# Optimization experiments

Hardware: AMD Instinct MI355X
Metric: run time of the kernel (lower is better)

The kernel has to match this reference:

```python
import jax, jax.numpy as jnp
import numpy as np

B, N, C, H = 8, 4096, 1024, 16
D = C // H  # head_dim = 64
EPS = 1e-12

def _l2norm(x):
    # F.normalize(x, p=2, dim=-1): x / max(||x||_2, eps)
    n = jnp.sqrt(jnp.sum(x * x, axis=-1, keepdims=True))
    return x / jnp.maximum(n, EPS)

def setup_inputs() -> dict:
    key = jax.random.key(0)
    ks = jax.random.split(key, 5)
    return {
        "x": jax.random.normal(ks[0], (B, N, C), dtype=jnp.float32),
        "qkv_w": jax.random.normal(ks[1], (C, 3 * C), dtype=jnp.float32) * 0.02,
        "qkv_b": jax.random.normal(ks[2], (3 * C,), dtype=jnp.float32) * 0.02,
        "proj_w": jax.random.normal(ks[3], (C, C), dtype=jnp.float32) * 0.02,
        "proj_b": jax.random.normal(ks[4], (C,), dtype=jnp.float32) * 0.02,
    }

def reference(x, qkv_w, qkv_b, proj_w, proj_b):
    b, n, c = x.shape
    qkv = (x @ qkv_w + qkv_b).reshape(b, n, 3, H, D)
    qkv = jnp.transpose(qkv, (2, 0, 3, 1, 4))  # [3,B,H,N,D]
    q, k, v = qkv[0], qkv[1], qkv[2]
    q = _l2norm(q)
    k = _l2norm(k)
    kv = jnp.einsum('bhnd,bhne->bhde', k, v)   # small [B,H,D,D] state
    out = jnp.einsum('bhnd,bhde->bhne', q, kv)  # [B,H,N,D]
    out = jnp.transpose(out, (0, 2, 1, 3)).reshape(b, n, c)
    return out @ proj_w + proj_b
```

## Files before the change

kernel.cpp:

```cpp
#include <hip/hip_runtime.h>
#include <stdint.h>

#define B_ 8
#define N_ 4096
#define C_ 1024
#define H_ 16
#define M_ (B_*N_)
#define BH_ (B_*H_)

typedef unsigned short u16;
typedef unsigned int   u32;
typedef __bf16 bf16x8 __attribute__((ext_vector_type(8)));
typedef float  f32x4  __attribute__((ext_vector_type(4)));

__device__ __forceinline__ u16 f2bf(float f) {
  union { float f; u32 u; } x; x.f = f;
  u32 r = x.u + 0x7fffu + ((x.u >> 16) & 1u);
  return (u16)(r >> 16);
}
__device__ __forceinline__ float bf2f(u16 b) {
  union { u32 u; float f; } x; x.u = ((u32)b) << 16;
  return x.f;
}
__device__ __forceinline__ void gload16(const void* g, void* l) {
  __builtin_amdgcn_global_load_lds(
      (const __attribute__((address_space(1))) void*)g,
      (__attribute__((address_space(3))) void*)l,
      16, 0, 0);
}
__device__ __forceinline__ void unpack8(uint4 r, float* f) {
  const u32 w[4] = {r.x, r.y, r.z, r.w};
#pragma unroll
  for (int i = 0; i < 4; ++i) {
    f[2*i]   = bf2f((u16)(w[i] & 0xffffu));
    f[2*i+1] = bf2f((u16)(w[i] >> 16));
  }
}
__device__ __forceinline__ uint4 pack8(const float* f) {
  uint4 r; u32* w = (u32*)&r;
#pragma unroll
  for (int i = 0; i < 4; ++i)
    w[i] = (u32)f2bf(f[2*i]) | ((u32)f2bf(f[2*i+1]) << 16);
  return r;
}

__global__ void cast_f32_bf16(const float* __restrict__ in, u16* __restrict__ out, int n4) {
  int i = blockIdx.x * blockDim.x + threadIdx.x;
  const int stride = gridDim.x * blockDim.x;
  for (; i < n4; i += stride) {
    float4 v = reinterpret_cast<const float4*>(in)[i];
    u32 lo = (u32)f2bf(v.x) | ((u32)f2bf(v.y) << 16);
    u32 hi = (u32)f2bf(v.z) | ((u32)f2bf(v.w) << 16);
    uint2 o; o.x = lo; o.y = hi;
    reinterpret_cast<uint2*>(out)[i] = o;
  }
}

__global__ void transpose_cast(const float* __restrict__ in, u16* __restrict__ out,
                               int R, int Cc) {
  __shared__ float t[32][33];
  const int bx = blockIdx.x * 32;
  const int by = blockIdx.y * 32;
  const int tx = threadIdx.x & 31;
  const int ty = threadIdx.x >> 5;
#pragma unroll
  for (int j = 0; j < 4; ++j) {
    const int r = by + ty + j * 8;
    t[ty + j * 8][tx] = in[(size_t)r * Cc + bx + tx];
  }
  __syncthreads();
#pragma unroll
  for (int j = 0; j < 4; ++j) {
    const int c = bx + ty + j * 8;
    out[(size_t)c * R + by + tx] = f2bf(t[tx][ty + j * 8]);
  }
}

template <int NC, bool OUT_BF16>
__global__ __launch_bounds__(512) void gemm256(const u16* __restrict__ A,
                                               const u16* __restrict__ Bt,
                                               const float* __restrict__ bias,
                                               void* __restrict__ outp,
                                               int K, int cpx) {
  __shared__ __align__(16) u16 As[2][256][64];
  __shared__ __align__(16) u16 Bs[2][256][64];
  const int tid  = threadIdx.x;
  const int lane = tid & 63;
  const int w    = tid >> 6;
  const int wm   = (w >> 2) & 1;
  const int wn   = w & 3;
  const int l15  = lane & 15;
  const int lk   = lane >> 4;

  const int bid = blockIdx.x;
  const int wg  = (bid & 7) * cpx + (bid >> 3);
  const size_t brow = (size_t)(wg & 127) * 256;
  const size_t bcol = (size_t)(wg >> 7) * 256;

  const int KT = K >> 6;
  f32x4 acc[2][2][4][2] = {};

  auto stage = [&](const u16* __restrict__ src, size_t rowbase, int kt,
                   u16* lds_tile, int h) {
#pragma unroll
    for (int is = 0; is < 2; ++is) {
      const int lin   = is * 8192 + tid * 16;
      const int row   = lin >> 7;
      const int chunk = ((lin >> 4) & 7) ^ (row & 7);
      gload16(src + (rowbase + (size_t)(h * 128 + row)) * K + kt * 64 + chunk * 8,
              (char*)lds_tile + h * 16384 + lin);
    }
  };
  auto fragA = [&](const u16* tb, int mh, int mf, int kc) -> bf16x8 {
    const int row   = mh * 128 + wm * 64 + mf * 16 + l15;
    const int chunk = ((kc << 2) | lk) ^ (row & 7);
    return *reinterpret_cast<const bf16x8*>((const char*)tb + row * 128 + chunk * 16);
  };
  auto fragB = [&](const u16* tb, int nh, int nf, int kc) -> bf16x8 {
    const int row   = nh * 128 + wn * 32 + nf * 16 + l15;
    const int chunk = ((kc << 2) | lk) ^ (row & 7);
    return *reinterpret_cast<const bf16x8*>((const char*)tb + row * 128 + chunk * 16);
  };

#define MFMA_Q(AF, BF, MH, NH) do {                                            \
    __builtin_amdgcn_s_barrier();                                              \
    __builtin_amdgcn_s_setprio(1);                                             \
    _Pragma("unroll") for (int mf = 0; mf < 4; ++mf)                           \
      _Pragma("unroll") for (int nf = 0; nf < 2; ++nf)                         \
        _Pragma("unroll") for (int kc = 0; kc < 2; ++kc)                       \
          acc[MH][NH][mf][nf] = __builtin_amdgcn_mfma_f32_16x16x32_bf16(       \
              AF[mf][kc], BF[nf][kc], acc[MH][NH][mf][nf], 0, 0, 0);           \
    __builtin_amdgcn_s_setprio(0);                                             \
    __builtin_amdgcn_s_barrier();                                              \
  } while (0)

  stage(A,  brow, 0, &As[0][0][0], 0);
  stage(Bt, bcol, 0, &Bs[0][0][0], 0);
  stage(A,  brow, 0, &As[0][0][0], 1);
  stage(Bt, bcol, 0, &Bs[0][0][0], 1);
  stage(A,  brow, 1, &As[1][0][0], 0);
  stage(Bt, bcol, 1, &Bs[1][0][0], 0);
  asm volatile("s_waitcnt vmcnt(4)" ::: "memory");
  __builtin_amdgcn_s_barrier();

  for (int t = 0; t < KT; ++t) {
    const u16* curA = &As[t & 1][0][0];
    const u16* curB = &Bs[t & 1][0][0];
    u16* nA  = &As[(t + 1) & 1][0][0];
    u16* nB  = &Bs[(t + 1) & 1][0][0];
    u16* n2A = &As[t & 1][0][0];
    u16* n2B = &Bs[t & 1][0][0];
    const bool s1 = (t + 1) < KT;
    const bool s2 = (t + 2) < KT;

    bf16x8 afA[4][2], afB[4][2], bf0[2][2], bf1[2][2];

#pragma unroll
    for (int mf = 0; mf < 4; ++mf)
#pragma unroll
      for (int kc = 0; kc < 2; ++kc) afA[mf][kc] = fragA(curA, 0, mf, kc);
#pragma unroll
    for (int nf = 0; nf < 2; ++nf)
#pragma unroll
      for (int kc = 0; kc < 2; ++kc) bf0[nf][kc] = fragB(curB, 0, nf, kc);
    if (s1) stage(A, brow, t + 1, nA, 1);
    MFMA_Q(afA, bf0, 0, 0);

#pragma unroll
    for (int nf = 0; nf < 2; ++nf)
#pragma unroll
      for (int kc = 0; kc < 2; ++kc) bf1[nf][kc] = fragB(curB, 1, nf, kc);
    if (s1) stage(Bt, bcol, t + 1, nB, 1);
    MFMA_Q(afA, bf1, 0, 1);

#pragma unroll
    for (int mf = 0; mf < 4; ++mf)
#pragma unroll
      for (int kc = 0; kc < 2; ++kc) afB[mf][kc] = fragA(curA, 1, mf, kc);
    if (s2) stage(A, brow, t + 2, n2A, 0);
    MFMA_Q(afB, bf1, 1, 1);

    if (s2) {
      stage(Bt, bcol, t + 2, n2B, 0);
      asm volatile("s_waitcnt vmcnt(4)" ::: "memory");
    } else {
      asm volatile("s_waitcnt vmcnt(0)" ::: "memory");
    }
    MFMA_Q(afB, bf0, 1, 0);
  }
#undef MFMA_Q

#pragma unroll
  for (int mh = 0; mh < 2; ++mh)
#pragma unroll
  for (int nh = 0; nh < 2; ++nh)
#pragma unroll
  for (int mf = 0; mf < 4; ++mf)
#pragma unroll
  for (int nf = 0; nf < 2; ++nf) {
    const size_t col = bcol + nh * 128 + wn * 32 + nf * 16 + l15;
    const float bv = bias[col];
    const size_t row0 = brow + mh * 128 + wm * 64 + mf * 16 + lk * 4;
#pragma unroll
    for (int r = 0; r < 4; ++r) {
      const float v = acc[mh][nh][mf][nf][r] + bv;
      if constexpr (OUT_BF16)
        ((u16*)outp)[(row0 + r) * NC + col] = f2bf(v);
      else
        ((float*)outp)[(row0 + r) * NC + col] = v;
    }
  }
}

__global__ void prep(u16* __restrict__ qkv, u16* __restrict__ KT, u16* __restrict__ VT) {
  const int bh = blockIdx.x, nt = blockIdx.y;
  const int b = bh >> 4, h = bh & 15;
  const int n0 = nt * 64;
  const int tid = threadIdx.x;
  __shared__ float tk[64 * 65];

#pragma unroll
  for (int it = 0; it < 2; ++it) {
    const int idx = it * 256 + tid;
    const int r = idx >> 3, c8 = idx & 7;
    const size_t addr = ((size_t)(b * N_ + n0 + r)) * 3072 + h * 64 + c8 * 8;
    uint4 raw = *reinterpret_cast<const uint4*>(qkv + addr);
    float f[8]; unpack8(raw, f);
    float ss = 0.f;
#pragma unroll
    for (int j = 0; j < 8; ++j) ss += f[j] * f[j];
    ss += __shfl_xor(ss, 1); ss += __shfl_xor(ss, 2); ss += __shfl_xor(ss, 4);
    const float sc = 1.f / fmaxf(sqrtf(ss), 1e-12f);
#pragma unroll
    for (int j = 0; j < 8; ++j) f[j] *= sc;
    *reinterpret_cast<uint4*>(qkv + addr) = pack8(f);
  }

#pragma unroll
  for (int it = 0; it < 2; ++it) {
    const int idx = it * 256 + tid;
    const int r = idx >> 3, c8 = idx & 7;
    const size_t addr = ((size_t)(b * N_ + n0 + r)) * 3072 + 1024 + h * 64 + c8 * 8;
    uint4 raw = *reinterpret_cast<const uint4*>(qkv + addr);
    float f[8]; unpack8(raw, f);
    float ss = 0.f;
#pragma unroll
    for (int j = 0; j < 8; ++j) ss += f[j] * f[j];
    ss += __shfl_xor(ss, 1); ss += __shfl_xor(ss, 2); ss += __shfl_xor(ss, 4);
    const float sc = 1.f / fmaxf(sqrtf(ss), 1e-12f);
#pragma unroll
    for (int j = 0; j < 8; ++j) tk[r * 65 + c8 * 8 + j] = f[j] * sc;
  }
  __syncthreads();
  {
    const int d = tid >> 2, nq = tid & 3;
    float v[16];
#pragma unroll
    for (int j = 0; j < 16; ++j) v[j] = tk[(nq * 16 + j) * 65 + d];
    u16* dst = KT + ((size_t)(bh * 64 + d)) * 4096 + n0 + nq * 16;
    *reinterpret_cast<uint4*>(dst)     = pack8(v);
    *reinterpret_cast<uint4*>(dst + 8) = pack8(v + 8);
  }
  __syncthreads();

#pragma unroll
  for (int it = 0; it < 2; ++it) {
    const int idx = it * 256 + tid;
    const int r = idx >> 3, c8 = idx & 7;
    const size_t addr = ((size_t)(b * N_ + n0 + r)) * 3072 + 2048 + h * 64 + c8 * 8;
    uint4 raw = *reinterpret_cast<const uint4*>(qkv + addr);
    float f[8]; unpack8(raw, f);
#pragma unroll
    for (int j = 0; j < 8; ++j) tk[r * 65 + c8 * 8 + j] = f[j];
  }
  __syncthreads();
  {
    const int e = tid >> 2, nq = tid & 3;
    float v[16];
#pragma unroll
    for (int j = 0; j < 16; ++j) v[j] = tk[(nq * 16 + j) * 65 + e];
    u16* dst = VT + ((size_t)(bh * 64 + e)) * 4096 + n0 + nq * 16;
    *reinterpret_cast<uint4*>(dst)     = pack8(v);
    *reinterpret_cast<uint4*>(dst + 8) = pack8(v + 8);
  }
}

__global__ void kv_gemm(const u16* __restrict__ VT, const u16* __restrict__ KT,
                        float* __restrict__ part) {
  const int bh = blockIdx.x, sp = blockIdx.y;
  __shared__ __align__(16) u16 Vs[64 * 64];
  __shared__ __align__(16) u16 Ks[64 * 64];
  const int tid  = threadIdx.x;
  const int lane = tid & 63;
  const int w    = tid >> 6;
  const int wm   = w >> 1, wn = w & 1;
  const int l15  = lane & 15;
  const int lk   = lane >> 4;

  f32x4 acc[2][2] = {};

  for (int kt = 0; kt < 16; ++kt) {
    const size_t k0 = (size_t)sp * 1024 + kt * 64;
#pragma unroll
    for (int is = 0; is < 2; ++is) {
      const int lin   = is * 4096 + tid * 16;
      const int row   = lin >> 7;
      const int chunk = ((lin >> 4) & 7) ^ (row & 7);
      gload16(VT + ((size_t)(bh * 64 + row)) * 4096 + k0 + chunk * 8, (char*)Vs + lin);
      gload16(KT + ((size_t)(bh * 64 + row)) * 4096 + k0 + chunk * 8, (char*)Ks + lin);
    }
    __syncthreads();
    bf16x8 fa[2][2], fb[2][2];
#pragma unroll
    for (int mf = 0; mf < 2; ++mf)
#pragma unroll
      for (int kc = 0; kc < 2; ++kc) {
        const int row = wm * 32 + mf * 16 + l15;
        const int chunk = ((kc << 2) | lk) ^ (row & 7);
        fa[mf][kc] = *reinterpret_cast<const bf16x8*>((const char*)Vs + row * 128 + chunk * 16);
      }
#pragma unroll
    for (int nf = 0; nf < 2; ++nf)
#pragma unroll
      for (int kc = 0; kc < 2; ++kc) {
        const int row = wn * 32 + nf * 16 + l15;
        const int chunk = ((kc << 2) | lk) ^ (row & 7);
        fb[nf][kc] = *reinterpret_cast<const bf16x8*>((const char*)Ks + row * 128 + chunk * 16);
      }
#pragma unroll
    for (int mf = 0; mf < 2; ++mf)
#pragma unroll
      for (int nf = 0; nf < 2; ++nf)
#pragma unroll
        for (int kc = 0; kc < 2; ++kc)
          acc[mf][nf] = __builtin_amdgcn_mfma_f32_16x16x32_bf16(
              fa[mf][kc], fb[nf][kc], acc[mf][nf], 0, 0, 0);
    __syncthreads();
  }

  float* base = part + ((size_t)sp * BH_ + bh) * 4096;
#pragma unroll
  for (int mf = 0; mf < 2; ++mf)
#pragma unroll
    for (int nf = 0; nf < 2; ++nf)
#pragma unroll
      for (int r = 0; r < 4; ++r) {
        const int e = wm * 32 + mf * 16 + lk * 4 + r;
        const int d = wn * 32 + nf * 16 + l15;
        base[e * 64 + d] = acc[mf][nf][r];
      }
}

__global__ void kv_reduce4(const float* __restrict__ part, u16* __restrict__ kvT) {
  const int i4 = (blockIdx.x * 256 + threadIdx.x) * 4;
  float4 s = *reinterpret_cast<const float4*>(part + i4);
#pragma unroll
  for (int sp = 1; sp < 4; ++sp) {
    float4 p = *reinterpret_cast<const float4*>(part + (size_t)sp * 524288 + i4);
    s.x += p.x; s.y += p.y; s.z += p.z; s.w += p.w;
  }
  u32 lo = (u32)f2bf(s.x) | ((u32)f2bf(s.y) << 16);
  u32 hi = (u32)f2bf(s.z) | ((u32)f2bf(s.w) << 16);
  uint2 o; o.x = lo; o.y = hi;
  *reinterpret_cast<uint2*>(kvT + i4) = o;
}

__global__ void attn_gemm(const u16* __restrict__ qkv, const u16* __restrict__ kvT,
                          u16* __restrict__ attn) {
  const int bh = blockIdx.x, nt = blockIdx.y;
  const int b = bh >> 4, h = bh & 15;
  const int n0 = nt * 128;
  __shared__ __align__(16) u16 Qs[128 * 64];
  __shared__ __align__(16) u16 Ks[64 * 64];
  const int tid  = threadIdx.x;
  const int lane = tid & 63;
  const int wm   = tid >> 6;
  const int l15  = lane & 15;
  const int lk   = lane >> 4;

#pragma unroll
  for (int is = 0; is < 4; ++is) {
    const int lin   = is * 4096 + tid * 16;
    const int row   = lin >> 7;
    const int chunk = ((lin >> 4) & 7) ^ (row & 7);
    gload16(qkv + ((size_t)(b * N_ + n0 + row)) * 3072 + h * 64 + chunk * 8,
            (char*)Qs + lin);
  }
#pragma unroll
  for (int is = 0; is < 2; ++is) {
    const int lin   = is * 4096 + tid * 16;
    const int row   = lin >> 7;
    const int chunk = ((lin >> 4) & 7) ^ (row & 7);
    gload16(kvT + (size_t)bh * 4096 + row * 64 + chunk * 8, (char*)Ks + lin);
  }
  __syncthreads();

  bf16x8 fq[2][2], fk[4][2];
#pragma unroll
  for (int mf = 0; mf < 2; ++mf)
#pragma unroll
    for (int kc = 0; kc < 2; ++kc) {
      const int row = wm * 32 + mf * 16 + l15;
      const int chunk = ((kc << 2) | lk) ^ (row & 7);
      fq[mf][kc] = *reinterpret_cast<const bf16x8*>((const char*)Qs + row * 128 + chunk * 16);
    }
#pragma unroll
  for (int nf = 0; nf < 4; ++nf)
#pragma unroll
    for (int kc = 0; kc < 2; ++kc) {
      const int row = nf * 16 + l15;
      const int chunk = ((kc << 2) | lk) ^ (row & 7);
      fk[nf][kc] = *reinterpret_cast<const bf16x8*>((const char*)Ks + row * 128 + chunk * 16);
    }
  f32x4 acc[2][4] = {};
#pragma unroll
  for (int mf = 0; mf < 2; ++mf)
#pragma unroll
    for (int nf = 0; nf < 4; ++nf)
#pragma unroll
      for (int kc = 0; kc < 2; ++kc)
        acc[mf][nf] = __builtin_amdgcn_mfma_f32_16x16x32_bf16(
            fq[mf][kc], fk[nf][kc], acc[mf][nf], 0, 0, 0);

#pragma unroll
  for (int mf = 0; mf < 2; ++mf)
#pragma unroll
    for (int nf = 0; nf < 4; ++nf)
#pragma unroll
      for (int r = 0; r < 4; ++r) {
        const size_t row = (size_t)(b * N_ + n0 + wm * 32 + mf * 16 + lk * 4 + r);
        attn[row * 1024 + h * 64 + nf * 16 + l15] = f2bf(acc[mf][nf][r]);
      }
}

#define WS_XB     0ull
#define WS_QKV    67108864ull
#define WS_VT     268435456ull
#define WS_WQKV   335544320ull
#define WS_WPROJ  341835776ull
#define WS_PART   343932928ull
#define WS_KVT    360710144ull

extern "C" void kernel_launch(void* const* d_in, const int* in_sizes, int n_in,
                              void* d_out, int out_size, void* d_ws, size_t ws_size,
                              hipStream_t stream) {
  const float* x      = (const float*)d_in[0];
  const float* qkv_w  = (const float*)d_in[1];
  const float* qkv_b  = (const float*)d_in[2];
  const float* proj_w = (const float*)d_in[3];
  const float* proj_b = (const float*)d_in[4];

  char* ws = (char*)d_ws;
  u16*   xb      = (u16*)(ws + WS_XB);
  u16*   KT      = (u16*)(ws + WS_XB);
  u16*   qkv     = (u16*)(ws + WS_QKV);
  u16*   VT      = (u16*)(ws + WS_VT);
  u16*   attn    = (u16*)(ws + WS_VT);
  u16*   wqkv_t  = (u16*)(ws + WS_WQKV);
  u16*   wproj_t = (u16*)(ws + WS_WPROJ);
  float* part    = (float*)(ws + WS_PART);
  u16*   kvT     = (u16*)(ws + WS_KVT);

  cast_f32_bf16<<<2048, 256, 0, stream>>>(x, xb, (M_ * C_) / 4);
  transpose_cast<<<dim3(96, 32), 256, 0, stream>>>(qkv_w, wqkv_t, 1024, 3072);
  transpose_cast<<<dim3(32, 32), 256, 0, stream>>>(proj_w, wproj_t, 1024, 1024);
  gemm256<3072, true><<<1536, 512, 0, stream>>>(xb, wqkv_t, qkv_b, qkv, 1024, 192);
  prep<<<dim3(128, 64), 256, 0, stream>>>(qkv, KT, VT);
  kv_gemm<<<dim3(128, 4), 256, 0, stream>>>(VT, KT, part);
  kv_reduce4<<<512, 256, 0, stream>>>(part, kvT);
  attn_gemm<<<dim3(128, 32), 256, 0, stream>>>(qkv, kvT, attn);
  gemm256<1024, false><<<512, 512, 0, stream>>>(attn, wproj_t, proj_b, d_out, 1024, 64);
}
```

Baseline: 505.2 us.

## Restructure GEMM main loop to prefetch full tile two steps ahead

Reorders the 256x256 bf16 GEMM's quadrant schedule so that each iteration stages all four halves of the k-tile two steps ahead, instead of splitting between t+1 and t+2. The next tile's B fragments are read early, and an explicit lgkmcnt(0) wait follows each barrier. The prologue loads two full tiles with a deeper vmcnt(6) wait, so more global loads are in flight behind MFMA work. The cost is tighter buffer-reuse ordering and more live fragment registers.

```diff
diff --git a/kernel.cpp b/kernel.cpp
--- a/kernel.cpp
+++ b/kernel.cpp
@@ -43,6 +43,9 @@
     w[i] = (u32)f2bf(f[2*i]) | ((u32)f2bf(f[2*i+1]) << 16);
   return r;
 }
+
+#define BAR   __builtin_amdgcn_s_barrier()
+#define LGKM0 asm volatile("s_waitcnt lgkmcnt(0)" ::: "memory")
 
 __global__ void cast_f32_bf16(const float* __restrict__ in, u16* __restrict__ out, int n4) {
   int i = blockIdx.x * blockDim.x + threadIdx.x;
@@ -97,7 +100,7 @@
   const size_t brow = (size_t)(wg & 127) * 256;
   const size_t bcol = (size_t)(wg >> 7) * 256;
 
-  const int KT = K >> 6;
+  const int KTn = K >> 6;
   f32x4 acc[2][2][4][2] = {};
 
   auto stage = [&](const u16* __restrict__ src, size_t rowbase, int kt,
@@ -122,8 +125,8 @@
     return *reinterpret_cast<const bf16x8*>((const char*)tb + row * 128 + chunk * 16);
   };
 
-#define MFMA_Q(AF, BF, MH, NH) do {                                            \
-    __builtin_amdgcn_s_barrier();                                              \
+#define MFMA16(AF, BF, MH, NH) do {                                            \
+    BAR; LGKM0;                                                                \
     __builtin_amdgcn_s_setprio(1);                                             \
     _Pragma("unroll") for (int mf = 0; mf < 4; ++mf)                           \
       _Pragma("unroll") for (int nf = 0; nf < 2; ++nf)                         \
@@ -131,64 +134,71 @@
           acc[MH][NH][mf][nf] = __builtin_amdgcn_mfma_f32_16x16x32_bf16(       \
               AF[mf][kc], BF[nf][kc], acc[MH][NH][mf][nf], 0, 0, 0);           \
     __builtin_amdgcn_s_setprio(0);                                             \
-    __builtin_amdgcn_s_barrier();                                              \
+    BAR;                                                                       \
   } while (0)
 
+  stage(Bt, bcol, 0, &Bs[0][0][0], 0);
   stage(A,  brow, 0, &As[0][0][0], 0);
-  stage(Bt, bcol, 0, &Bs[0][0][0], 0);
   stage(A,  brow, 0, &As[0][0][0], 1);
   stage(Bt, bcol, 0, &Bs[0][0][0], 1);
+  stage(Bt, bcol, 1, &Bs[1][0][0], 0);
   stage(A,  brow, 1, &As[1][0][0], 0);
-  stage(Bt, bcol, 1, &Bs[1][0][0], 0);
-  asm volatile("s_waitcnt vmcnt(4)" ::: "memory");
-  __builtin_amdgcn_s_barrier();
-
-  for (int t = 0; t < KT; ++t) {
-    const u16* curA = &As[t & 1][0][0];
-    const u16* curB = &Bs[t & 1][0][0];
-    u16* nA  = &As[(t + 1) & 1][0][0];
-    u16* nB  = &Bs[(t + 1) & 1][0][0];
-    u16* n2A = &As[t & 1][0][0];
-    u16* n2B = &Bs[t & 1][0][0];
-    const bool s1 = (t + 1) < KT;
-    const bool s2 = (t + 2) < KT;
-
-    bf16x8 afA[4][2], afB[4][2], bf0[2][2], bf1[2][2];
+  stage(A,  brow, 1, &As[1][0][0], 1);
+  stage(Bt, bcol, 1, &Bs[1][0][0], 1);
+  asm volatile("s_waitcnt vmcnt(6)" ::: "memory");
+  BAR;
+
+  bf16x8 a0[4][2], a1[4][2], b0[2][2], b1[2][2];
+#pragma unroll
+  for (int nf = 0; nf < 2; ++nf)
+#pragma unroll
+    for (int kc = 0; kc < 2; ++kc) b0[nf][kc] = fragB(&Bs[0][0][0], 0, nf, kc);
+
+  for (int t = 0; t < KTn; ++t) {
+    const u16* cA = &As[t & 1][0][0];
+    const u16* cB = &Bs[t & 1][0][0];
+    const u16* nB = &Bs[(t + 1) & 1][0][0];
+    u16* sA = &As[t & 1][0][0];
+    u16* sB = &Bs[t & 1][0][0];
+    const bool s1 = (t + 1) < KTn;
+    const bool s2 = (t + 2) < KTn;
 
 #pragma unroll
     for (int mf = 0; mf < 4; ++mf)
 #pragma unroll
-      for (int kc = 0; kc < 2; ++kc) afA[mf][kc] = fragA(curA, 0, mf, kc);
+      for (int kc = 0; kc < 2; ++kc) a0[mf][kc] = fragA(cA, 0, mf, kc);
+    if (s2) stage(Bt, bcol, t + 2, sB, 0);
+    MFMA16(a0, b0, 0, 0);
+
+#pragma unroll
+    for (int mf = 0; mf < 4; ++mf)
+#pragma unroll
+      for (int kc = 0; kc < 2; ++kc) a1[mf][kc] = fragA(cA, 1, mf, kc);
+    if (s2) stage(A, brow, t + 2, sA, 0);
+    MFMA16(a1, b0, 1, 0);
+
 #pragma unroll
     for (int nf = 0; nf < 2; ++nf)
 #pragma unroll
-      for (int kc = 0; kc < 2; ++kc) bf0[nf][kc] = fragB(curB, 0, nf, kc);
-    if (s1) stage(A, brow, t + 1, nA, 1);
-    MFMA_Q(afA, bf0, 0, 0);
-
-#pragma unroll
-    for (int nf = 0; nf < 2; ++nf)
-#pragma unroll
-      for (int kc = 0; kc < 2; ++kc) bf1[nf][kc] = fragB(curB, 1, nf, kc);
-    if (s1) stage(Bt, bcol, t + 1, nB, 1);
-    MFMA_Q(afA, bf1, 0, 1);
-
-#pragma unroll
-    for (int mf = 0; mf < 4; ++mf)
-#pragma unroll
-      for (int kc = 0; kc < 2; ++kc) afB[mf][kc] = fragA(curA, 1, mf, kc);
-    if (s2) stage(A, brow, t + 2, n2A, 0);
-    MFMA_Q(afB, bf1, 1, 1);
-
+      for (int kc = 0; kc < 2; ++kc) b1[nf][kc] = fragB(cB, 1, nf, kc);
+    if (s2) stage(A, brow, t + 2, sA, 1);
+    MFMA16(a1, b1, 1, 1);
+
+    if (s1) {
+#pragma unroll
+      for (int nf = 0; nf < 2; ++nf)
+#pragma unroll
+        for (int kc = 0; kc < 2; ++kc) b0[nf][kc] = fragB(nB, 0, nf, kc);
+    }
     if (s2) {
-      stage(Bt, bcol, t + 2, n2B, 0);
-      asm volatile("s_waitcnt vmcnt(4)" ::: "memory");
+      stage(Bt, bcol, t + 2, sB, 1);
+      asm volatile("s_waitcnt vmcnt(6)" ::: "memory");
     } else {
       asm volatile("s_waitcnt vmcnt(0)" ::: "memory");
     }
-    MFMA_Q(afB, bf0, 1, 0);
-  }
-#undef MFMA_Q
+    MFMA16(a0, b1, 0, 1);
+  }
+#undef MFMA16
 
 #pragma unroll
   for (int mh = 0; mh < 2; ++mh)
```

New measurement: 601.8 us. 1.19x slower.

## Fuse K-normalize and transpose into kv GEMM, defer Q norm to attn epilogue

Applied to the files above, without the earlier changes.

Removes the prep kernel that wrote normalized Q back and materialized transposed K and V. The kv GEMM now reads K and V straight from qkv, normalizes K in registers, and stages both through fp32 shared memory. A small kernel computes per-row Q inverse norms, which attn_gemm applies as a per-row scale on its output. The split over N goes from 4 to 8 with a matching reduce. This cuts the extra global round trips, but the MFMA fragments are now built from strided fp32 shared-memory reads instead of vector bf16 loads, and there is no async prefetch.

```diff
diff --git a/kernel.cpp b/kernel.cpp
--- a/kernel.cpp
+++ b/kernel.cpp
@@ -42,6 +42,10 @@
   for (int i = 0; i < 4; ++i)
     w[i] = (u32)f2bf(f[2*i]) | ((u32)f2bf(f[2*i+1]) << 16);
   return r;
+}
+__device__ __forceinline__ bf16x8 packbf8(const float* f) {
+  uint4 p = pack8(f);
+  return *reinterpret_cast<bf16x8*>(&p);
 }
 
 __global__ void cast_f32_bf16(const float* __restrict__ in, u16* __restrict__ out, int n4) {
@@ -212,84 +216,25 @@
   }
 }
 
-__global__ void prep(u16* __restrict__ qkv, u16* __restrict__ KT, u16* __restrict__ VT) {
-  const int bh = blockIdx.x, nt = blockIdx.y;
+__global__ void qsc_kernel(const u16* __restrict__ qkv, float* __restrict__ qsc) {
+  const int t = threadIdx.x;
+  const size_t p = (size_t)blockIdx.x * 32 + (t >> 3);
+  const int c8 = t & 7;
+  const size_t row = p >> 4;
+  const int h = (int)(p & 15);
+  uint4 raw = *reinterpret_cast<const uint4*>(qkv + row * 3072 + h * 64 + c8 * 8);
+  float f[8]; unpack8(raw, f);
+  float ss = 0.f;
+#pragma unroll
+  for (int j = 0; j < 8; ++j) ss += f[j] * f[j];
+  ss += __shfl_xor(ss, 1); ss += __shfl_xor(ss, 2); ss += __shfl_xor(ss, 4);
+  if (c8 == 0) qsc[p] = 1.f / fmaxf(sqrtf(ss), 1e-12f);
+}
+
+__global__ __launch_bounds__(256) void kv_fused(const u16* __restrict__ qkv,
+                                                float* __restrict__ part) {
+  const int bh = blockIdx.x, sp = blockIdx.y;
   const int b = bh >> 4, h = bh & 15;
-  const int n0 = nt * 64;
-  const int tid = threadIdx.x;
-  __shared__ float tk[64 * 65];
-
-#pragma unroll
-  for (int it = 0; it < 2; ++it) {
-    const int idx = it * 256 + tid;
-    const int r = idx >> 3, c8 = idx & 7;
-    const size_t addr = ((size_t)(b * N_ + n0 + r)) * 3072 + h * 64 + c8 * 8;
-    uint4 raw = *reinterpret_cast<const uint4*>(qkv + addr);
-    float f[8]; unpack8(raw, f);
-    float ss = 0.f;
-#pragma unroll
-    for (int j = 0; j < 8; ++j) ss += f[j] * f[j];
-    ss += __shfl_xor(ss, 1); ss += __shfl_xor(ss, 2); ss += __shfl_xor(ss, 4);
-    const float sc = 1.f / fmaxf(sqrtf(ss), 1e-12f);
-#pragma unroll
-    for (int j = 0; j < 8; ++j) f[j] *= sc;
-    *reinterpret_cast<uint4*>(qkv + addr) = pack8(f);
-  }
-
-#pragma unroll
-  for (int it = 0; it < 2; ++it) {
-    const int idx = it * 256 + tid;
-    const int r = idx >> 3, c8 = idx & 7;
-    const size_t addr = ((size_t)(b * N_ + n0 + r)) * 3072 + 1024 + h * 64 + c8 * 8;
-    uint4 raw = *reinterpret_cast<const uint4*>(qkv + addr);
-    float f[8]; unpack8(raw, f);
-    float ss = 0.f;
-#pragma unroll
-    for (int j = 0; j < 8; ++j) ss += f[j] * f[j];
-    ss += __shfl_xor(ss, 1); ss += __shfl_xor(ss, 2); ss += __shfl_xor(ss, 4);
-    const float sc = 1.f / fmaxf(sqrtf(ss), 1e-12f);
-#pragma unroll
-    for (int j = 0; j < 8; ++j) tk[r * 65 + c8 * 8 + j] = f[j] * sc;
-  }
-  __syncthreads();
-  {
-    const int d = tid >> 2, nq = tid & 3;
-    float v[16];
-#pragma unroll
-    for (int j = 0; j < 16; ++j) v[j] = tk[(nq * 16 + j) * 65 + d];
-    u16* dst = KT + ((size_t)(bh * 64 + d)) * 4096 + n0 + nq * 16;
-    *reinterpret_cast<uint4*>(dst)     = pack8(v);
-    *reinterpret_cast<uint4*>(dst + 8) = pack8(v + 8);
-  }
-  __syncthreads();
-
-#pragma unroll
-  for (int it = 0; it < 2; ++it) {
-    const int idx = it * 256 + tid;
-    const int r = idx >> 3, c8 = idx & 7;
-    const size_t addr = ((size_t)(b * N_ + n0 + r)) * 3072 + 2048 + h * 64 + c8 * 8;
-    uint4 raw = *reinterpret_cast<const uint4*>(qkv + addr);
-    float f[8]; unpack8(raw, f);
-#pragma unroll
-    for (int j = 0; j < 8; ++j) tk[r * 65 + c8 * 8 + j] = f[j];
-  }
-  __syncthreads();
-  {
-    const int e = tid >> 2, nq = tid & 3;
-    float v[16];
-#pragma unroll
-    for (int j = 0; j < 16; ++j) v[j] = tk[(nq * 16 + j) * 65 + e];
-    u16* dst = VT + ((size_t)(bh * 64 + e)) * 4096 + n0 + nq * 16;
-    *reinterpret_cast<uint4*>(dst)     = pack8(v);
-    *reinterpret_cast<uint4*>(dst + 8) = pack8(v + 8);
-  }
-}
-
-__global__ void kv_gemm(const u16* __restrict__ VT, const u16* __restrict__ KT,
-                        float* __restrict__ part) {
-  const int bh = blockIdx.x, sp = blockIdx.y;
-  __shared__ __align__(16) u16 Vs[64 * 64];
-  __shared__ __align__(16) u16 Ks[64 * 64];
   const int tid  = threadIdx.x;
   const int lane = tid & 63;
   const int w    = tid >> 6;
@@ -297,35 +242,55 @@
   const int l15  = lane & 15;
   const int lk   = lane >> 4;
 
+  __shared__ float Ks[64 * 65];
+  __shared__ float Vs[64 * 65];
+
   f32x4 acc[2][2] = {};
-
-  for (int kt = 0; kt < 16; ++kt) {
-    const size_t k0 = (size_t)sp * 1024 + kt * 64;
-#pragma unroll
-    for (int is = 0; is < 2; ++is) {
-      const int lin   = is * 4096 + tid * 16;
-      const int row   = lin >> 7;
-      const int chunk = ((lin >> 4) & 7) ^ (row & 7);
-      gload16(VT + ((size_t)(bh * 64 + row)) * 4096 + k0 + chunk * 8, (char*)Vs + lin);
-      gload16(KT + ((size_t)(bh * 64 + row)) * 4096 + k0 + chunk * 8, (char*)Ks + lin);
-    }
+  const size_t nbase = (size_t)b * N_ + (size_t)sp * 512;
+
+  for (int ch = 0; ch < 8; ++ch) {
     __syncthreads();
+#pragma unroll
+    for (int it = 0; it < 2; ++it) {
+      const int idx = it * 256 + tid;
+      const int r = idx >> 3, c8 = idx & 7;
+      const size_t rowoff = (nbase + (size_t)(ch * 64 + r)) * 3072 + h * 64 + c8 * 8;
+      uint4 kraw = *reinterpret_cast<const uint4*>(qkv + rowoff + 1024);
+      float kf[8]; unpack8(kraw, kf);
+      float ss = 0.f;
+#pragma unroll
+      for (int j = 0; j < 8; ++j) ss += kf[j] * kf[j];
+      ss += __shfl_xor(ss, 1); ss += __shfl_xor(ss, 2); ss += __shfl_xor(ss, 4);
+      const float sc = 1.f / fmaxf(sqrtf(ss), 1e-12f);
+#pragma unroll
+      for (int j = 0; j < 8; ++j) Ks[r * 65 + c8 * 8 + j] = kf[j] * sc;
+      uint4 vraw = *reinterpret_cast<const uint4*>(qkv + rowoff + 2048);
+      float vf[8]; unpack8(vraw, vf);
+#pragma unroll
+      for (int j = 0; j < 8; ++j) Vs[r * 65 + c8 * 8 + j] = vf[j];
+    }
+    __syncthreads();
+
     bf16x8 fa[2][2], fb[2][2];
 #pragma unroll
     for (int mf = 0; mf < 2; ++mf)
 #pragma unroll
       for (int kc = 0; kc < 2; ++kc) {
-        const int row = wm * 32 + mf * 16 + l15;
-        const int chunk = ((kc << 2) | lk) ^ (row & 7);
-        fa[mf][kc] = *reinterpret_cast<const bf16x8*>((const char*)Vs + row * 128 + chunk * 16);
+        const int e = wm * 32 + mf * 16 + l15;
+        float tmp[8];
+#pragma unroll
+        for (int j = 0; j < 8; ++j) tmp[j] = Vs[(kc * 32 + lk * 8 + j) * 65 + e];
+        fa[mf][kc] = packbf8(tmp);
       }
 #pragma unroll
     for (int nf = 0; nf < 2; ++nf)
 #pragma unroll
       for (int kc = 0; kc < 2; ++kc) {
-        const int row = wn * 32 + nf * 16 + l15;
-        const int chunk = ((kc << 2) | lk) ^ (row & 7);
-        fb[nf][kc] = *reinterpret_cast<const bf16x8*>((const char*)Ks + row * 128 + chunk * 16);
+        const int d = wn * 32 + nf * 16 + l15;
+        float tmp[8];
+#pragma unroll
+        for (int j = 0; j < 8; ++j) tmp[j] = Ks[(kc * 32 + lk * 8 + j) * 65 + d];
+        fb[nf][kc] = packbf8(tmp);
       }
 #pragma unroll
     for (int mf = 0; mf < 2; ++mf)
@@ -335,7 +300,6 @@
         for (int kc = 0; kc < 2; ++kc)
           acc[mf][nf] = __builtin_amdgcn_mfma_f32_16x16x32_bf16(
               fa[mf][kc], fb[nf][kc], acc[mf][nf], 0, 0, 0);
-    __syncthreads();
   }
 
   float* base = part + ((size_t)sp * BH_ + bh) * 4096;
@@ -351,11 +315,11 @@
       }
 }
 
-__global__ void kv_reduce4(const float* __restrict__ part, u16* __restrict__ kvT) {
+__global__ void kv_reduce8(const float* __restrict__ part, u16* __restrict__ kvT) {
   const int i4 = (blockIdx.x * 256 + threadIdx.x) * 4;
   float4 s = *reinterpret_cast<const float4*>(part + i4);
 #pragma unroll
-  for (int sp = 1; sp < 4; ++sp) {
+  for (int sp = 1; sp < 8; ++sp) {
     float4 p = *reinterpret_cast<const float4*>(part + (size_t)sp * 524288 + i4);
     s.x += p.x; s.y += p.y; s.z += p.z; s.w += p.w;
   }
@@ -366,7 +330,7 @@
 }
 
 __global__ void attn_gemm(const u16* __restrict__ qkv, const u16* __restrict__ kvT,
-                          u16* __restrict__ attn) {
+                          const float* __restrict__ qsc, u16* __restrict__ attn) {
   const int bh = blockIdx.x, nt = blockIdx.y;
   const int b = bh >> 4, h = bh & 15;
   const int n0 = nt * 128;
@@ -425,12 +389,13 @@
 #pragma unroll
   for (int mf = 0; mf < 2; ++mf)
 #pragma unroll
-    for (int nf = 0; nf < 4; ++nf)
-#pragma unroll
-      for (int r = 0; r < 4; ++r) {
-        const size_t row = (size_t)(b * N_ + n0 + wm * 32 + mf * 16 + lk * 4 + r);
-        attn[row * 1024 + h * 64 + nf * 16 + l15] = f2bf(acc[mf][nf][r]);
-      }
+    for (int r = 0; r < 4; ++r) {
+      const size_t row = (size_t)(b * N_ + n0 + wm * 32 + mf * 16 + lk * 4 + r);
+      const float sc = qsc[row * 16 + h];
+#pragma unroll
+      for (int nf = 0; nf < 4; ++nf)
+        attn[row * 1024 + h * 64 + nf * 16 + l15] = f2bf(acc[mf][nf][r] * sc);
+    }
 }
 
 #define WS_XB     0ull
@@ -438,7 +403,7 @@
 #define WS_VT     268435456ull
 #define WS_WQKV   335544320ull
 #define WS_WPROJ  341835776ull
-#define WS_PART   343932928ull
+#define WS_QSC    343932928ull
 #define WS_KVT    360710144ull
 
 extern "C" void kernel_launch(void* const* d_in, const int* in_sizes, int n_in,
@@ -452,22 +417,21 @@
 
   char* ws = (char*)d_ws;
   u16*   xb      = (u16*)(ws + WS_XB);
-  u16*   KT      = (u16*)(ws + WS_XB);
   u16*   qkv     = (u16*)(ws + WS_QKV);
-  u16*   VT      = (u16*)(ws + WS_VT);
+  float* part    = (float*)(ws + WS_VT);
   u16*   attn    = (u16*)(ws + WS_VT);
   u16*   wqkv_t  = (u16*)(ws + WS_WQKV);
   u16*   wproj_t = (u16*)(ws + WS_WPROJ);
-  float* part    = (float*)(ws + WS_PART);
+  float* qsc     = (float*)(ws + WS_QSC);
   u16*   kvT     = (u16*)(ws + WS_KVT);
 
   cast_f32_bf16<<<2048, 256, 0, stream>>>(x, xb, (M_ * C_) / 4);
   transpose_cast<<<dim3(96, 32), 256, 0, stream>>>(qkv_w, wqkv_t, 1024, 3072);
   transpose_cast<<<dim3(32, 32), 256, 0, stream>>>(proj_w, wproj_t, 1024, 1024);
   gemm256<3072, true><<<1536, 512, 0, stream>>>(xb, wqkv_t, qkv_b, qkv, 1024, 192);
-  prep<<<dim3(128, 64), 256, 0, stream>>>(qkv, KT, VT);
-  kv_gemm<<<dim3(128, 4), 256, 0, stream>>>(VT, KT, part);
-  kv_reduce4<<<512, 256, 0, stream>>>(part, kvT);
-  attn_gemm<<<dim3(128, 32), 256, 0, stream>>>(qkv, kvT, attn);
+  qsc_kernel<<<16384, 256, 0, stream>>>(qkv, qsc);
+  kv_fused<<<dim3(128, 8), 256, 0, stream>>>(qkv, part);
+  kv_reduce8<<<512, 256, 0, stream>>>(part, kvT);
+  attn_gemm<<<dim3(128, 32), 256, 0, stream>>>(qkv, kvT, qsc, attn);
   gemm256<1024, false><<<512, 512, 0, stream>>>(attn, wproj_t, proj_b, d_out, 1024, 64);
 }
```

Result: faster. 452.8 us (-10.4%).
